# Optimization experiments

Measured on AMD Instinct MI355X. Metric: run time of the kernel, lower is better.

The kernel has to match this reference:

```python
import jax, jax.numpy as jnp
import numpy as np

IMG = 224
PATCH = 16
CH = 3
D_DIM = 768
ROW = IMG // PATCH            # 14
N_PATCHES = ROW * ROW         # 196
PATCH_DIM = PATCH * PATCH * CH  # 768


def setup_inputs() -> dict:
    key = jax.random.key(0)
    k1, k2, k3 = jax.random.split(key, 3)
    x = jax.random.normal(k1, (32, CH, IMG, IMG), dtype=jnp.float32)
    # stacked per-patch Linear weights: torch nn.Linear(in=PATCH_DIM, out=D_DIM)
    # weight shape [out, in]; we store [n_patches, in, out] for batched einsum
    bound = 1.0 / np.sqrt(PATCH_DIM)
    W = jax.random.uniform(k2, (N_PATCHES, PATCH_DIM, D_DIM), dtype=jnp.float32,
                           minval=-bound, maxval=bound)
    b = jax.random.uniform(k3, (N_PATCHES, D_DIM), dtype=jnp.float32,
                           minval=-bound, maxval=bound)
    return {"x": x, "W": W, "b": b}


def _extract_patches(x):
    # x: [B, C, H, W] -> [B, n_patches, C*p*p] matching torch crop+Flatten order
    B = x.shape[0]
    x = x.reshape(B, CH, ROW, PATCH, ROW, PATCH)          # [B,C,r,p,c,p]
    x = x.transpose(0, 2, 4, 1, 3, 5)                     # [B,r,c,C,p,p]
    return x.reshape(B, N_PATCHES, PATCH_DIM)


def reference(x, W, b):
    patches = _extract_patches(x)                         # [B, N, P]
    # per-patch independent linear: one batched GEMM over the patch axis
    out = jnp.einsum('bnp,npd->bnd', patches, W) + b      # [B, N, D]
    return out
```

## Files before the change

kernel.cpp:

```cpp
#include <hip/hip_runtime.h>

#define IMG 224
#define PATCHSZ 16
#define CHN 3
#define DDIM 768
#define ROWN 14
#define NPATCH 196
#define PDIM 768
#define BATCH 32

#define DTILE 256
#define KCHUNK 64
#define NCHUNK (PDIM / KCHUNK)
#define KSUB 16
#define NSUB (PDIM / KSUB)

__global__ void extract_patches_kernel(const float* __restrict__ x,
                                       float* __restrict__ P) {
    int i = blockIdx.x * blockDim.x + threadIdx.x;
    if (i >= NPATCH * BATCH * PDIM) return;
    int k  = i % PDIM;
    int nb = i / PDIM;
    int b  = nb % BATCH;
    int n  = nb / BATCH;
    int ch = k >> 8;
    int py = (k >> 4) & 15;
    int px = k & 15;
    int r = n / ROWN, c = n % ROWN;
    P[i] = x[(((size_t)b * CHN + ch) * IMG + r * PATCHSZ + py) * IMG
             + c * PATCHSZ + px];
}

#define ACC_ROW(i, pv, wj)                                                   \
    acc[i][0] = fmaf(pv, wj.x, acc[i][0]);                                   \
    acc[i][1] = fmaf(pv, wj.y, acc[i][1]);                                   \
    acc[i][2] = fmaf(pv, wj.z, acc[i][2]);                                   \
    acc[i][3] = fmaf(pv, wj.w, acc[i][3]);

__global__ __launch_bounds__(256, 2) void patch_gemm_kernel(
    const float* __restrict__ P,
    const float* __restrict__ W,
    const float* __restrict__ bias,
    float* __restrict__ out)
{
    __shared__ __align__(16) float wt[2][KSUB][DTILE];
    __shared__ __align__(16) float ap[2][KCHUNK][BATCH];

    const int blk  = blockIdx.x;
    const int n    = blk / 3;
    const int dblk = blk % 3;
    const int tid  = threadIdx.x;
    const int ln   = tid & 63;
    const int wv   = tid >> 6;
    const int b0   = wv * 8;
    const int d    = dblk * DTILE + ln * 4;

    const float* Wn0 = W + (size_t)n * PDIM * DDIM + dblk * DTILE;
    const float* Pn  = P + (size_t)n * BATCH * PDIM;

    const int sb = tid >> 3;
    const int sk = (tid & 7) * 8;

    float acc[8][4];
#pragma unroll
    for (int i = 0; i < 8; ++i)
#pragma unroll
        for (int j = 0; j < 4; ++j) acc[i][j] = 0.f;

    auto issueW = [&](int u) {
        const float* src = Wn0 + (size_t)u * KSUB * DDIM;
        float* dst = &wt[u & 1][0][0];
#pragma unroll
        for (int j = 0; j < 4; ++j) {
            const int row = wv * 4 + j;
            __builtin_amdgcn_global_load_lds(
                (const __attribute__((address_space(1))) unsigned int*)
                    (src + (size_t)row * DDIM + ln * 4),
                (__attribute__((address_space(3))) unsigned int*)
                    (dst + row * DTILE + ln * 4),
                16, 0, 0);
        }
    };

    {
        const float* s = Pn + (size_t)sb * PDIM + sk;
        float4 v0 = *reinterpret_cast<const float4*>(s);
        float4 v1 = *reinterpret_cast<const float4*>(s + 4);
        float (*apb)[BATCH] = ap[0];
        apb[sk + 0][sb] = v0.x; apb[sk + 1][sb] = v0.y;
        apb[sk + 2][sb] = v0.z; apb[sk + 3][sb] = v0.w;
        apb[sk + 4][sb] = v1.x; apb[sk + 5][sb] = v1.y;
        apb[sk + 6][sb] = v1.z; apb[sk + 7][sb] = v1.w;
    }
    float4 pn0, pn1;
    {
        const float* s = Pn + (size_t)sb * PDIM + KCHUNK + sk;
        pn0 = *reinterpret_cast<const float4*>(s);
        pn1 = *reinterpret_cast<const float4*>(s + 4);
    }
    issueW(0);

#pragma unroll 1
    for (int u = 0; u < NSUB; ++u) {
        __syncthreads();
        if (u + 1 < NSUB) issueW(u + 1);

        const int c  = u >> 2;
        const int kb = (u & 3) * KSUB;
        const float* wbuf = &wt[u & 1][0][0] + ln * 4;
        const float* pbuf = &ap[c & 1][0][0] + b0;

#pragma unroll 4
        for (int kk = 0; kk < KSUB; ++kk) {
            float4 w = *reinterpret_cast<const float4*>(wbuf + kk * DTILE);
            const float* pp = pbuf + (size_t)(kb + kk) * BATCH;
            float4 p01 = *reinterpret_cast<const float4*>(pp);
            float4 p23 = *reinterpret_cast<const float4*>(pp + 4);
            ACC_ROW(0, p01.x, w) ACC_ROW(1, p01.y, w)
            ACC_ROW(2, p01.z, w) ACC_ROW(3, p01.w, w)
            ACC_ROW(4, p23.x, w) ACC_ROW(5, p23.y, w)
            ACC_ROW(6, p23.z, w) ACC_ROW(7, p23.w, w)
        }

        if ((u & 3) == 3 && c + 1 < NCHUNK) {
            float (*apb)[BATCH] = ap[(c + 1) & 1];
            apb[sk + 0][sb] = pn0.x; apb[sk + 1][sb] = pn0.y;
            apb[sk + 2][sb] = pn0.z; apb[sk + 3][sb] = pn0.w;
            apb[sk + 4][sb] = pn1.x; apb[sk + 5][sb] = pn1.y;
            apb[sk + 6][sb] = pn1.z; apb[sk + 7][sb] = pn1.w;
            if (c + 2 < NCHUNK) {
                const float* s = Pn + (size_t)sb * PDIM + (c + 2) * KCHUNK + sk;
                pn0 = *reinterpret_cast<const float4*>(s);
                pn1 = *reinterpret_cast<const float4*>(s + 4);
            }
        }
    }

    float4 bv = *reinterpret_cast<const float4*>(bias + (size_t)n * DDIM + d);
#pragma unroll
    for (int i = 0; i < 8; ++i) {
        const int b = b0 + i;
        float4 o;
        o.x = acc[i][0] + bv.x;
        o.y = acc[i][1] + bv.y;
        o.z = acc[i][2] + bv.z;
        o.w = acc[i][3] + bv.w;
        *reinterpret_cast<float4*>(out + ((size_t)b * NPATCH + n) * DDIM + d) = o;
    }
}

extern "C" void kernel_launch(void* const* d_in, const int* in_sizes, int n_in,
                              void* d_out, int out_size, void* d_ws, size_t ws_size,
                              hipStream_t stream) {
    const float* x    = (const float*)d_in[0];
    const float* W    = (const float*)d_in[1];
    const float* bias = (const float*)d_in[2];
    float* out = (float*)d_out;
    float* P   = (float*)d_ws;

    int total = NPATCH * BATCH * PDIM;
    extract_patches_kernel<<<(total + 255) / 256, 256, 0, stream>>>(x, P);
    patch_gemm_kernel<<<NPATCH * 3, 256, 0, stream>>>(P, W, bias, out);
}
```

Before: 164.3 us.

## Fuse patch extraction into GEMM loads and double the W sub-tile depth

Drops the separate patch-extraction kernel and its workspace buffer. The GEMM now computes image addresses directly, gathering each 8-float segment from x (8 contiguous pixels within one patch row). This removes a full write and re-read of the patch matrix plus one kernel launch. KSUB also grows from 16 to 32, which halves the number of barrier iterations but doubles the per-stage W LDS buffer and may reduce occupancy.

```diff
diff --git a/kernel.cpp b/kernel.cpp
--- a/kernel.cpp
+++ b/kernel.cpp
@@ -10,26 +10,11 @@
 #define BATCH 32
 
 #define DTILE 256
+#define NDBLK (DDIM / DTILE)
 #define KCHUNK 64
 #define NCHUNK (PDIM / KCHUNK)
-#define KSUB 16
+#define KSUB 32
 #define NSUB (PDIM / KSUB)
-
-__global__ void extract_patches_kernel(const float* __restrict__ x,
-                                       float* __restrict__ P) {
-    int i = blockIdx.x * blockDim.x + threadIdx.x;
-    if (i >= NPATCH * BATCH * PDIM) return;
-    int k  = i % PDIM;
-    int nb = i / PDIM;
-    int b  = nb % BATCH;
-    int n  = nb / BATCH;
-    int ch = k >> 8;
-    int py = (k >> 4) & 15;
-    int px = k & 15;
-    int r = n / ROWN, c = n % ROWN;
-    P[i] = x[(((size_t)b * CHN + ch) * IMG + r * PATCHSZ + py) * IMG
-             + c * PATCHSZ + px];
-}
 
 #define ACC_ROW(i, pv, wj)                                                   \
     acc[i][0] = fmaf(pv, wj.x, acc[i][0]);                                   \
@@ -38,7 +23,7 @@
     acc[i][3] = fmaf(pv, wj.w, acc[i][3]);
 
 __global__ __launch_bounds__(256, 2) void patch_gemm_kernel(
-    const float* __restrict__ P,
+    const float* __restrict__ x,
     const float* __restrict__ W,
     const float* __restrict__ bias,
     float* __restrict__ out)
@@ -47,8 +32,8 @@
     __shared__ __align__(16) float ap[2][KCHUNK][BATCH];
 
     const int blk  = blockIdx.x;
-    const int n    = blk / 3;
-    const int dblk = blk % 3;
+    const int n    = blk / NDBLK;
+    const int dblk = blk % NDBLK;
     const int tid  = threadIdx.x;
     const int ln   = tid & 63;
     const int wv   = tid >> 6;
@@ -56,10 +41,19 @@
     const int d    = dblk * DTILE + ln * 4;
 
     const float* Wn0 = W + (size_t)n * PDIM * DDIM + dblk * DTILE;
-    const float* Pn  = P + (size_t)n * BATCH * PDIM;
 
     const int sb = tid >> 3;
     const int sk = (tid & 7) * 8;
+    const int rr = n / ROWN, cc = n % ROWN;
+
+    auto xsrc = [&](int c) {
+        int k0 = c * KCHUNK + sk;
+        int ch = k0 >> 8;
+        int py = (k0 >> 4) & 15;
+        int px = k0 & 15;
+        return x + (((size_t)sb * CHN + ch) * IMG + (rr * PATCHSZ + py)) * IMG
+                 + cc * PATCHSZ + px;
+    };
 
     float acc[8][4];
 #pragma unroll
@@ -71,8 +65,8 @@
         const float* src = Wn0 + (size_t)u * KSUB * DDIM;
         float* dst = &wt[u & 1][0][0];
 #pragma unroll
-        for (int j = 0; j < 4; ++j) {
-            const int row = wv * 4 + j;
+        for (int j = 0; j < 8; ++j) {
+            const int row = wv * 8 + j;
             __builtin_amdgcn_global_load_lds(
                 (const __attribute__((address_space(1))) unsigned int*)
                     (src + (size_t)row * DDIM + ln * 4),
@@ -83,9 +77,9 @@
     };
 
     {
-        const float* s = Pn + (size_t)sb * PDIM + sk;
-        float4 v0 = *reinterpret_cast<const float4*>(s);
-        float4 v1 = *reinterpret_cast<const float4*>(s + 4);
+        const float* xs = xsrc(0);
+        float4 v0 = *reinterpret_cast<const float4*>(xs);
+        float4 v1 = *reinterpret_cast<const float4*>(xs + 4);
         float (*apb)[BATCH] = ap[0];
         apb[sk + 0][sb] = v0.x; apb[sk + 1][sb] = v0.y;
         apb[sk + 2][sb] = v0.z; apb[sk + 3][sb] = v0.w;
@@ -94,9 +88,9 @@
     }
     float4 pn0, pn1;
     {
-        const float* s = Pn + (size_t)sb * PDIM + KCHUNK + sk;
-        pn0 = *reinterpret_cast<const float4*>(s);
-        pn1 = *reinterpret_cast<const float4*>(s + 4);
+        const float* xs = xsrc(1);
+        pn0 = *reinterpret_cast<const float4*>(xs);
+        pn1 = *reinterpret_cast<const float4*>(xs + 4);
     }
     issueW(0);
 
@@ -105,8 +99,8 @@
         __syncthreads();
         if (u + 1 < NSUB) issueW(u + 1);
 
-        const int c  = u >> 2;
-        const int kb = (u & 3) * KSUB;
+        const int c  = u >> 1;
+        const int kb = (u & 1) * KSUB;
         const float* wbuf = &wt[u & 1][0][0] + ln * 4;
         const float* pbuf = &ap[c & 1][0][0] + b0;
 
@@ -122,16 +116,16 @@
             ACC_ROW(6, p23.z, w) ACC_ROW(7, p23.w, w)
         }
 
-        if ((u & 3) == 3 && c + 1 < NCHUNK) {
+        if ((u & 1) == 1 && c + 1 < NCHUNK) {
             float (*apb)[BATCH] = ap[(c + 1) & 1];
             apb[sk + 0][sb] = pn0.x; apb[sk + 1][sb] = pn0.y;
             apb[sk + 2][sb] = pn0.z; apb[sk + 3][sb] = pn0.w;
             apb[sk + 4][sb] = pn1.x; apb[sk + 5][sb] = pn1.y;
             apb[sk + 6][sb] = pn1.z; apb[sk + 7][sb] = pn1.w;
             if (c + 2 < NCHUNK) {
-                const float* s = Pn + (size_t)sb * PDIM + (c + 2) * KCHUNK + sk;
-                pn0 = *reinterpret_cast<const float4*>(s);
-                pn1 = *reinterpret_cast<const float4*>(s + 4);
+                const float* xs = xsrc(c + 2);
+                pn0 = *reinterpret_cast<const float4*>(xs);
+                pn1 = *reinterpret_cast<const float4*>(xs + 4);
             }
         }
     }
@@ -156,9 +150,6 @@
     const float* W    = (const float*)d_in[1];
     const float* bias = (const float*)d_in[2];
     float* out = (float*)d_out;
-    float* P   = (float*)d_ws;
 
-    int total = NPATCH * BATCH * PDIM;
-    extract_patches_kernel<<<(total + 255) / 256, 256, 0, stream>>>(x, P);
-    patch_gemm_kernel<<<NPATCH * 3, 256, 0, stream>>>(P, W, bias, out);
+    patch_gemm_kernel<<<NPATCH * NDBLK, 256, 0, stream>>>(x, W, bias, out);
 }
```

Result: slower. 179.0 us (+8.9%).

## Triple-buffer weight tiles with manual vmcnt waits instead of syncthreads

Applied to the files above, without the earlier changes.

Weight sub-tiles now use a three-slot LDS ring, with loads issued two stages ahead. The full __syncthreads is replaced by explicit s_waitcnt on lgkmcnt/vmcnt plus a raw s_barrier, so only the oldest in-flight async load has to finish before each step. The next patch-chunk register prefetch is moved to the start of each chunk to hide its latency. This aims to keep more global-to-LDS traffic in flight on a GEMM bound by weight bandwidth. The cost is extra LDS use, which may reduce occupancy, and correctness depends on the hand-counted vmcnt values.

```diff
diff --git a/kernel.cpp b/kernel.cpp
--- a/kernel.cpp
+++ b/kernel.cpp
@@ -10,6 +10,7 @@
 #define BATCH 32
 
 #define DTILE 256
+#define NDBLK (DDIM / DTILE)
 #define KCHUNK 64
 #define NCHUNK (PDIM / KCHUNK)
 #define KSUB 16
@@ -43,12 +44,12 @@
     const float* __restrict__ bias,
     float* __restrict__ out)
 {
-    __shared__ __align__(16) float wt[2][KSUB][DTILE];
+    __shared__ __align__(16) float wt[3][KSUB][DTILE];
     __shared__ __align__(16) float ap[2][KCHUNK][BATCH];
 
     const int blk  = blockIdx.x;
-    const int n    = blk / 3;
-    const int dblk = blk % 3;
+    const int n    = blk / NDBLK;
+    const int dblk = blk % NDBLK;
     const int tid  = threadIdx.x;
     const int ln   = tid & 63;
     const int wv   = tid >> 6;
@@ -67,9 +68,9 @@
 #pragma unroll
         for (int j = 0; j < 4; ++j) acc[i][j] = 0.f;
 
-    auto issueW = [&](int u) {
+    auto issueW = [&](int u, int slot) {
         const float* src = Wn0 + (size_t)u * KSUB * DDIM;
-        float* dst = &wt[u & 1][0][0];
+        float* dst = &wt[slot][0][0];
 #pragma unroll
         for (int j = 0; j < 4; ++j) {
             const int row = wv * 4 + j;
@@ -92,22 +93,34 @@
         apb[sk + 4][sb] = v1.x; apb[sk + 5][sb] = v1.y;
         apb[sk + 6][sb] = v1.z; apb[sk + 7][sb] = v1.w;
     }
+    issueW(0, 0);
+    issueW(1, 1);
+
     float4 pn0, pn1;
-    {
-        const float* s = Pn + (size_t)sb * PDIM + KCHUNK + sk;
-        pn0 = *reinterpret_cast<const float4*>(s);
-        pn1 = *reinterpret_cast<const float4*>(s + 4);
-    }
-    issueW(0);
+    int rd = 0;
 
 #pragma unroll 1
-    for (int u = 0; u < NSUB; ++u) {
-        __syncthreads();
-        if (u + 1 < NSUB) issueW(u + 1);
+    for (int v = 0; v < NSUB; ++v) {
+        asm volatile("s_waitcnt lgkmcnt(0)" ::: "memory");
+        if (v == NSUB - 1) {
+            asm volatile("s_waitcnt vmcnt(0)" ::: "memory");
+        } else {
+            asm volatile("s_waitcnt vmcnt(4)" ::: "memory");
+        }
+        __builtin_amdgcn_s_barrier();
 
-        const int c  = u >> 2;
-        const int kb = (u & 3) * KSUB;
-        const float* wbuf = &wt[u & 1][0][0] + ln * 4;
+        int wr = rd + 2; if (wr >= 3) wr -= 3;
+        if (v + 2 < NSUB) issueW(v + 2, wr);
+
+        const int c  = v >> 2;
+        if ((v & 3) == 0 && c + 1 < NCHUNK) {
+            const float* s = Pn + (size_t)sb * PDIM + (c + 1) * KCHUNK + sk;
+            pn0 = *reinterpret_cast<const float4*>(s);
+            pn1 = *reinterpret_cast<const float4*>(s + 4);
+        }
+
+        const int kb = (v & 3) * KSUB;
+        const float* wbuf = &wt[rd][0][0] + ln * 4;
         const float* pbuf = &ap[c & 1][0][0] + b0;
 
 #pragma unroll 4
@@ -122,18 +135,15 @@
             ACC_ROW(6, p23.z, w) ACC_ROW(7, p23.w, w)
         }
 
-        if ((u & 3) == 3 && c + 1 < NCHUNK) {
+        if ((v & 3) == 3 && c + 1 < NCHUNK) {
             float (*apb)[BATCH] = ap[(c + 1) & 1];
             apb[sk + 0][sb] = pn0.x; apb[sk + 1][sb] = pn0.y;
             apb[sk + 2][sb] = pn0.z; apb[sk + 3][sb] = pn0.w;
             apb[sk + 4][sb] = pn1.x; apb[sk + 5][sb] = pn1.y;
             apb[sk + 6][sb] = pn1.z; apb[sk + 7][sb] = pn1.w;
-            if (c + 2 < NCHUNK) {
-                const float* s = Pn + (size_t)sb * PDIM + (c + 2) * KCHUNK + sk;
-                pn0 = *reinterpret_cast<const float4*>(s);
-                pn1 = *reinterpret_cast<const float4*>(s + 4);
-            }
         }
+
+        rd = (rd == 2) ? 0 : rd + 1;
     }
 
     float4 bv = *reinterpret_cast<const float4*>(bias + (size_t)n * DDIM + d);
@@ -160,5 +170,5 @@
 
     int total = NPATCH * BATCH * PDIM;
     extract_patches_kernel<<<(total + 255) / 256, 256, 0, stream>>>(x, P);
-    patch_gemm_kernel<<<NPATCH * 3, 256, 0, stream>>>(P, W, bias, out);
+    patch_gemm_kernel<<<NPATCH * NDBLK, 256, 0, stream>>>(P, W, bias, out);
 }
```

Result: slower. 210.3 us (+28.0%).
